# Kernel optimization log

Hardware: AMD Instinct MI355X
Metric: run time of the kernel (lower is better)

## Reference

```python
import jax, jax.numpy as jnp
import numpy as np

T, B, D, H = 256, 64, 1024, 1024  # seq_len, batch, input_dim, hidden_dim (= n_qubits)


def setup_inputs() -> dict:
    key = jax.random.key(0)
    ks = jax.random.split(key, 9)
    scale = 1.0 / np.sqrt(D + H)
    inp = {
        "inputs": jax.random.normal(ks[0], (T, B, D), dtype=jnp.float32),
        # nn.Linear weights (out=H wires, in=D+H) and biases, per gate
        "Wf": jax.random.normal(ks[1], (H, D + H), dtype=jnp.float32) * scale,
        "bf": jnp.zeros((H,), dtype=jnp.float32),
        "gbf": jnp.zeros((H,), dtype=jnp.float32),  # QLinearGate bias (init zeros)
        "Wi": jax.random.normal(ks[2], (H, D + H), dtype=jnp.float32) * scale,
        "bi": jnp.zeros((H,), dtype=jnp.float32),
        "gbi": jnp.zeros((H,), dtype=jnp.float32),
        "Wu": jax.random.normal(ks[3], (H, D + H), dtype=jnp.float32) * scale,
        "bu": jnp.zeros((H,), dtype=jnp.float32),
        "gbu": jnp.zeros((H,), dtype=jnp.float32),
        "Wo": jax.random.normal(ks[4], (H, D + H), dtype=jnp.float32) * scale,
        "bo": jnp.zeros((H,), dtype=jnp.float32),
        "gbo": jnp.zeros((H,), dtype=jnp.float32),
    }
    return inp


def reference(inputs, Wf, bf, gbf, Wi, bi, gbi, Wu, bu, gbu, Wo, bo, gbo):
    # QLinearGate: RY(theta)|0> -> <Z> = cos(theta); matmul with identity; add bias.
    def qgate(z, gb):
        return jnp.cos(z) + gb

    def step(carry, x):
        hx, cx = carry
        comb = jnp.concatenate([x, hx], axis=1)  # (B, D+H)
        f = jax.nn.sigmoid(qgate(comb @ Wf.T + bf, gbf))
        i = jax.nn.sigmoid(qgate(comb @ Wi.T + bi, gbi))
        g = jnp.tanh(qgate(comb @ Wu.T + bu, gbu))
        o = jax.nn.sigmoid(qgate(comb @ Wo.T + bo, gbo))
        cx = f * cx + i * g
        hx = o * jnp.tanh(cx)
        return (hx, cx), hx

    Bdim = inputs.shape[1]
    init = (jnp.zeros((Bdim, H), inputs.dtype), jnp.zeros((Bdim, H), inputs.dtype))
    (hx, cx), outputs = jax.lax.scan(step, init, inputs)
    return outputs, (hx, cx)
```

## Files before the change

kernel.cpp:

```cpp
#include <hip/hip_runtime.h>
#include <cmath>
#include <cstring>

constexpr int TT = 256;
constexpr int BB = 64;
constexpr int DD = 1024;
constexpr int HH = 1024;
constexpr int KK = DD + HH;
constexpr int NBLK = 256;
constexpr int NTHR = 512;
constexpr int CK = 64;
constexpr int NCHF = KK / CK;
constexpr int HPB = 4;

constexpr int WS_UINTS = TT * 8 * 16 + TT * 16;

__device__ __forceinline__ float sigm(float v) { return 1.0f / (1.0f + expf(-v)); }

__device__ __forceinline__ float qsum4(float x) {
  int v = __builtin_amdgcn_mov_dpp(__float_as_int(x), 0xB1, 0xF, 0xF, true);
  x += __int_as_float(v);
  v = __builtin_amdgcn_mov_dpp(__float_as_int(x), 0x4E, 0xF, 0xF, true);
  x += __int_as_float(v);
  return x;
}

__device__ __forceinline__ void gridbar(unsigned* ws, int t, int tid, int bid) {
  __syncthreads();
  if (tid == 0) {
    asm volatile("s_waitcnt vmcnt(0)" ::: "memory");
    unsigned* grp  = ws + (size_t)(t * 8 + (bid >> 5)) * 16;
    unsigned* done = ws + 32768 + (size_t)t * 16;
    unsigned old = __hip_atomic_fetch_add(grp, 1u, __ATOMIC_RELAXED, __HIP_MEMORY_SCOPE_AGENT);
    if (old == 31u)
      __hip_atomic_fetch_add(done, 1u, __ATOMIC_RELAXED, __HIP_MEMORY_SCOPE_AGENT);
    while (__hip_atomic_load(done, __ATOMIC_RELAXED, __HIP_MEMORY_SCOPE_AGENT) < 8u)
      __builtin_amdgcn_s_sleep(1);
    asm volatile("" ::: "memory");
  }
  __syncthreads();
}

__global__ void zero_ws(unsigned* p, int n) {
  int i = blockIdx.x * blockDim.x + threadIdx.x;
  if (i < n) p[i] = 0u;
}

__global__ __launch_bounds__(NTHR, 2)
void qlstm_fused3(const float* __restrict__ x,
                  const float* __restrict__ Wf, const float* __restrict__ bf, const float* __restrict__ gbf,
                  const float* __restrict__ Wi, const float* __restrict__ bi, const float* __restrict__ gbi,
                  const float* __restrict__ Wu, const float* __restrict__ bu, const float* __restrict__ gbu,
                  const float* __restrict__ Wo, const float* __restrict__ bo, const float* __restrict__ gbo,
                  float* __restrict__ out, unsigned* __restrict__ ws)
{
  __shared__ float lds[40960];
  float* const Wl   = lds;
  float* const cbA  = lds + 32768;
  float* const cbB  = lds + 36864;
  float* const zbuf = lds + 32768;

  const int tid  = threadIdx.x;
  const int lane = tid & 63;
  const int rg   = tid >> 6;
  const int cgp  = lane >> 4;
  const int kp   = lane & 15;
  const int srow = tid >> 3;
  const int sseg = tid & 7;
  const int bid  = blockIdx.x;
  const int h0   = bid * HPB;

  {
    const float* Wg[4] = {Wf, Wi, Wu, Wo};
    #pragma unroll
    for (int j = 0; j < 16; ++j) {
      const float4 w = *(const float4*)(Wg[j >> 2] + (size_t)(h0 + (j & 3)) * KK + tid * 4);
      *(float4*)&Wl[j * KK + tid * 4] = w;
    }
  }

  const int urow = tid >> 2;
  const int uhl  = tid & 3;
  const int hcell = h0 + uhl;
  float bfv = 0, gbfv = 0, biv = 0, gbiv = 0, buv = 0, gbuv = 0, bov = 0, gbov = 0;
  if (tid < 256) {
    bfv = bf[hcell]; gbfv = gbf[hcell];
    biv = bi[hcell]; gbiv = gbi[hcell];
    buv = bu[hcell]; gbuv = gbu[hcell];
    bov = bo[hcell]; gbov = gbo[hcell];
  }
  float cx = 0.0f, hxl = 0.0f;

  auto ld8 = [](const float* p) -> float2 {
    unsigned long long u = __hip_atomic_load((const unsigned long long*)(const void*)p,
                                             __ATOMIC_RELAXED, __HIP_MEMORY_SCOPE_AGENT);
    float2 r; __builtin_memcpy(&r, &u, 8); return r;
  };

  for (int t = 0; t < TT; ++t) {
    const int nch = (t == 0) ? (DD / CK) : NCHF;

    float acc[8][4];
    #pragma unroll
    for (int i = 0; i < 8; ++i)
      #pragma unroll
      for (int j = 0; j < 4; ++j) acc[i][j] = 0.0f;

    auto loadChunk = [&](int kc, float4& va, float4& vb) {
      const int k0 = kc * CK;
      if (k0 < DD) {
        const float* base = x + (size_t)t * BB * DD + (size_t)srow * DD + k0;
        va = *(const float4*)(base + sseg * 4);
        vb = *(const float4*)(base + 32 + sseg * 4);
      } else {
        const float* base = out + (size_t)(t - 1) * BB * HH + (size_t)srow * HH + (k0 - DD);
        const float2 a0 = ld8(base + sseg * 4);
        const float2 a1 = ld8(base + sseg * 4 + 2);
        const float2 b0 = ld8(base + 32 + sseg * 4);
        const float2 b1 = ld8(base + 32 + sseg * 4 + 2);
        va = {a0.x, a0.y, a1.x, a1.y};
        vb = {b0.x, b0.y, b1.x, b1.y};
      }
    };
    auto storeChunk = [&](float* cb, const float4 va, const float4 vb) {
      *(float4*)&cb[srow * CK + sseg * 4]      = va;
      *(float4*)&cb[srow * CK + 32 + sseg * 4] = vb;
    };

    float4 va, vb;
    loadChunk(0, va, vb);
    storeChunk(cbA, va, vb);
    loadChunk(1, va, vb);

    for (int kc = 0; kc < nch; ++kc) {
      float* const cbW = (kc & 1) ? cbA : cbB;
      float* const cbR = (kc & 1) ? cbB : cbA;
      if (kc + 1 < nch) storeChunk(cbW, va, vb);
      if (kc + 2 < nch) loadChunk(kc + 2, va, vb);

      const int cko = kc * CK;
      float4 cfr[8];
      #pragma unroll
      for (int i = 0; i < 8; ++i)
        cfr[i] = *(const float4*)&cbR[(rg * 8 + i) * CK + kp * 4];
      #pragma unroll
      for (int j = 0; j < 4; ++j) {
        const float4 w = *(const float4*)&Wl[(cgp * 4 + j) * KK + cko + kp * 4];
        #pragma unroll
        for (int i = 0; i < 8; ++i) {
          acc[i][j] = fmaf(cfr[i].x, w.x, acc[i][j]);
          acc[i][j] = fmaf(cfr[i].y, w.y, acc[i][j]);
          acc[i][j] = fmaf(cfr[i].z, w.z, acc[i][j]);
          acc[i][j] = fmaf(cfr[i].w, w.w, acc[i][j]);
        }
      }
    }

    #pragma unroll
    for (int i = 0; i < 8; ++i)
      #pragma unroll
      for (int j = 0; j < 4; ++j) acc[i][j] = qsum4(acc[i][j]);

    __syncthreads();
    if ((lane & 3) == 0) {
      const int kpg = (lane >> 2) & 3;
      #pragma unroll
      for (int i = 0; i < 8; ++i) {
        const float4 v = {acc[i][0], acc[i][1], acc[i][2], acc[i][3]};
        *(float4*)&zbuf[(size_t)((kpg * 64) + rg * 8 + i) * 16 + cgp * 4] = v;
      }
    }
    __syncthreads();

    if (tid < 256) {
      float zf = bfv, zi = biv, zu = buv, zo = bov;
      #pragma unroll
      for (int p = 0; p < 4; ++p) {
        const float* zr = &zbuf[(size_t)(p * 64 + urow) * 16];
        zf += zr[0 + uhl];
        zi += zr[4 + uhl];
        zu += zr[8 + uhl];
        zo += zr[12 + uhl];
      }
      const float fg = sigm(cosf(zf) + gbfv);
      const float ig = sigm(cosf(zi) + gbiv);
      const float gg = tanhf(cosf(zu) + gbuv);
      const float og = sigm(cosf(zo) + gbov);
      cx = fg * cx + ig * gg;
      const float hx = og * tanhf(cx);
      __hip_atomic_store(&out[(size_t)t * BB * HH + (size_t)urow * HH + hcell], hx,
                         __ATOMIC_RELAXED, __HIP_MEMORY_SCOPE_AGENT);
      hxl = hx;
    }

    gridbar(ws, t, tid, bid);
  }

  if (tid < 256) {
    float* hxout = out + (size_t)TT * BB * HH;
    float* cxout = hxout + (size_t)BB * HH;
    hxout[(size_t)urow * HH + hcell] = hxl;
    cxout[(size_t)urow * HH + hcell] = cx;
  }
}

extern "C" void kernel_launch(void* const* d_in, const int* in_sizes, int n_in,
                              void* d_out, int out_size, void* d_ws, size_t ws_size,
                              hipStream_t stream) {
  const float* x   = (const float*)d_in[0];
  const float* Wf  = (const float*)d_in[1];
  const float* bf_ = (const float*)d_in[2];
  const float* gbf = (const float*)d_in[3];
  const float* Wi  = (const float*)d_in[4];
  const float* bi_ = (const float*)d_in[5];
  const float* gbi = (const float*)d_in[6];
  const float* Wu  = (const float*)d_in[7];
  const float* bu_ = (const float*)d_in[8];
  const float* gbu = (const float*)d_in[9];
  const float* Wo  = (const float*)d_in[10];
  const float* bo_ = (const float*)d_in[11];
  const float* gbo = (const float*)d_in[12];
  float* out = (float*)d_out;
  unsigned* wsp = (unsigned*)d_ws;

  zero_ws<<<(WS_UINTS + 255) / 256, 256, 0, stream>>>(wsp, WS_UINTS);

  void* args[] = {&x, &Wf, &bf_, &gbf, &Wi, &bi_, &gbi, &Wu, &bu_, &gbu,
                  &Wo, &bo_, &gbo, &out, &wsp};
  hipLaunchCooperativeKernel((void*)qlstm_fused3, dim3(NBLK), dim3(NTHR),
                             args, 0, stream);
}
```

Measured before the change: 5.489 ms.

## Switch gate matmuls to split-bf16 MFMA with segmented input projection

Replaces the scalar FP32 FMA loop with bf16 MFMA 16x16x32 instructions. Weights and activations are split into hi and lo bf16 parts and combined with three MFMAs to keep accuracy close to FP32. Weights are stored swizzled in LDS. The input projection for 8 timesteps is computed ahead of the recurrent part and parked in workspace, so each barrier-separated step only does the hidden-state half of the K dimension. The cost is a larger LDS footprint (136 KB), which likely allows only one block per CU, plus extra workspace traffic and bf16-split rounding error.

```diff
diff --git a/kernel.cpp b/kernel.cpp
--- a/kernel.cpp
+++ b/kernel.cpp
@@ -6,23 +6,26 @@
 constexpr int BB = 64;
 constexpr int DD = 1024;
 constexpr int HH = 1024;
-constexpr int KK = DD + HH;
+constexpr int KK = 2048;
 constexpr int NBLK = 256;
 constexpr int NTHR = 512;
-constexpr int CK = 64;
-constexpr int NCHF = KK / CK;
+constexpr int SEG = 8;
+constexpr int NSEG = TT / SEG;
 constexpr int HPB = 4;
 
-constexpr int WS_UINTS = TT * 8 * 16 + TT * 16;
+constexpr int FLAG_UINTS = TT * 8 * 16 + TT * 16;
+
+typedef __attribute__((ext_vector_type(8))) short bf16x8;
+typedef __attribute__((ext_vector_type(4))) float f32x4;
 
 __device__ __forceinline__ float sigm(float v) { return 1.0f / (1.0f + expf(-v)); }
 
-__device__ __forceinline__ float qsum4(float x) {
-  int v = __builtin_amdgcn_mov_dpp(__float_as_int(x), 0xB1, 0xF, 0xF, true);
-  x += __int_as_float(v);
-  v = __builtin_amdgcn_mov_dpp(__float_as_int(x), 0x4E, 0xF, 0xF, true);
-  x += __int_as_float(v);
-  return x;
+__device__ __forceinline__ void split2(float c, short& hi, short& lo) {
+  unsigned u  = __float_as_uint(c);
+  unsigned uh = u & 0xFFFF0000u;
+  hi = (short)(uh >> 16);
+  float r = c - __uint_as_float(uh);
+  lo = (short)(__float_as_uint(r) >> 16);
 }
 
 __device__ __forceinline__ void gridbar(unsigned* ws, int t, int tid, int bid) {
@@ -47,35 +50,42 @@
 }
 
 __global__ __launch_bounds__(NTHR, 2)
-void qlstm_fused3(const float* __restrict__ x,
-                  const float* __restrict__ Wf, const float* __restrict__ bf, const float* __restrict__ gbf,
-                  const float* __restrict__ Wi, const float* __restrict__ bi, const float* __restrict__ gbi,
-                  const float* __restrict__ Wu, const float* __restrict__ bu, const float* __restrict__ gbu,
-                  const float* __restrict__ Wo, const float* __restrict__ bo, const float* __restrict__ gbo,
-                  float* __restrict__ out, unsigned* __restrict__ ws)
+void qlstm_mfma5(const float* __restrict__ x,
+                 const float* __restrict__ Wf, const float* __restrict__ bf, const float* __restrict__ gbf,
+                 const float* __restrict__ Wi, const float* __restrict__ bi, const float* __restrict__ gbi,
+                 const float* __restrict__ Wu, const float* __restrict__ bu, const float* __restrict__ gbu,
+                 const float* __restrict__ Wo, const float* __restrict__ bo, const float* __restrict__ gbo,
+                 float* __restrict__ out, unsigned* __restrict__ ws)
 {
-  __shared__ float lds[40960];
-  float* const Wl   = lds;
-  float* const cbA  = lds + 32768;
-  float* const cbB  = lds + 36864;
-  float* const zbuf = lds + 32768;
+  __shared__ __attribute__((aligned(16))) char smem[139264];
+  char*  const Whi  = smem;
+  char*  const Wlo  = smem + 65536;
+  float* const zbuf = (float*)(smem + 131072);
 
   const int tid  = threadIdx.x;
   const int lane = tid & 63;
-  const int rg   = tid >> 6;
-  const int cgp  = lane >> 4;
-  const int kp   = lane & 15;
-  const int srow = tid >> 3;
-  const int sseg = tid & 7;
+  const int wid  = tid >> 6;
+  const int m    = wid & 3;
+  const int p    = wid >> 2;
+  const int arow = lane & 15;
+  const int kseg = lane >> 4;
+  const int col  = lane & 15;
   const int bid  = blockIdx.x;
   const int h0   = bid * HPB;
 
+  float* const wsz = (float*)ws + FLAG_UINTS;
+
   {
     const float* Wg[4] = {Wf, Wi, Wu, Wo};
-    #pragma unroll
-    for (int j = 0; j < 16; ++j) {
-      const float4 w = *(const float4*)(Wg[j >> 2] + (size_t)(h0 + (j & 3)) * KK + tid * 4);
-      *(float4*)&Wl[j * KK + tid * 4] = w;
+    for (int u = tid; u < 4096; u += NTHR) {
+      const int c = u >> 8, s = u & 255;
+      const float* src = Wg[c >> 2] + (size_t)(h0 + (c & 3)) * KK + s * 8;
+      bf16x8 h8, l8;
+      #pragma unroll
+      for (int j = 0; j < 8; ++j) { short h, l; split2(src[j], h, l); h8[j] = h; l8[j] = l; }
+      const int addr = (c * 4096 + s * 16) ^ ((c & 7) << 4);
+      *(bf16x8*)(Whi + addr) = h8;
+      *(bf16x8*)(Wlo + addr) = l8;
     }
   }
 
@@ -91,109 +101,99 @@
   }
   float cx = 0.0f, hxl = 0.0f;
 
-  auto ld8 = [](const float* p) -> float2 {
-    unsigned long long u = __hip_atomic_load((const unsigned long long*)(const void*)p,
+  auto ld8 = [](const float* ptr) -> float2 {
+    unsigned long long u = __hip_atomic_load((const unsigned long long*)(const void*)ptr,
                                              __ATOMIC_RELAXED, __HIP_MEMORY_SCOPE_AGENT);
     float2 r; __builtin_memcpy(&r, &u, 8); return r;
   };
 
-  for (int t = 0; t < TT; ++t) {
-    const int nch = (t == 0) ? (DD / CK) : NCHF;
-
-    float acc[8][4];
+  auto kstep = [&](const float c[8], int kglob, f32x4& acc) {
+    bf16x8 ahi, alo;
     #pragma unroll
-    for (int i = 0; i < 8; ++i)
-      #pragma unroll
-      for (int j = 0; j < 4; ++j) acc[i][j] = 0.0f;
-
-    auto loadChunk = [&](int kc, float4& va, float4& vb) {
-      const int k0 = kc * CK;
-      if (k0 < DD) {
-        const float* base = x + (size_t)t * BB * DD + (size_t)srow * DD + k0;
-        va = *(const float4*)(base + sseg * 4);
-        vb = *(const float4*)(base + 32 + sseg * 4);
-      } else {
-        const float* base = out + (size_t)(t - 1) * BB * HH + (size_t)srow * HH + (k0 - DD);
-        const float2 a0 = ld8(base + sseg * 4);
-        const float2 a1 = ld8(base + sseg * 4 + 2);
-        const float2 b0 = ld8(base + 32 + sseg * 4);
-        const float2 b1 = ld8(base + 32 + sseg * 4 + 2);
-        va = {a0.x, a0.y, a1.x, a1.y};
-        vb = {b0.x, b0.y, b1.x, b1.y};
-      }
-    };
-    auto storeChunk = [&](float* cb, const float4 va, const float4 vb) {
-      *(float4*)&cb[srow * CK + sseg * 4]      = va;
-      *(float4*)&cb[srow * CK + 32 + sseg * 4] = vb;
-    };
-
-    float4 va, vb;
-    loadChunk(0, va, vb);
-    storeChunk(cbA, va, vb);
-    loadChunk(1, va, vb);
-
-    for (int kc = 0; kc < nch; ++kc) {
-      float* const cbW = (kc & 1) ? cbA : cbB;
-      float* const cbR = (kc & 1) ? cbB : cbA;
-      if (kc + 1 < nch) storeChunk(cbW, va, vb);
-      if (kc + 2 < nch) loadChunk(kc + 2, va, vb);
-
-      const int cko = kc * CK;
-      float4 cfr[8];
-      #pragma unroll
-      for (int i = 0; i < 8; ++i)
-        cfr[i] = *(const float4*)&cbR[(rg * 8 + i) * CK + kp * 4];
-      #pragma unroll
-      for (int j = 0; j < 4; ++j) {
-        const float4 w = *(const float4*)&Wl[(cgp * 4 + j) * KK + cko + kp * 4];
+    for (int j = 0; j < 8; ++j) { short h, l; split2(c[j], h, l); ahi[j] = h; alo[j] = l; }
+    const int ad = (col * 4096 + (kglob + kseg * 8) * 2) ^ ((col & 7) << 4);
+    const bf16x8 bhi = *(const bf16x8*)(Whi + ad);
+    const bf16x8 blo = *(const bf16x8*)(Wlo + ad);
+    acc = __builtin_amdgcn_mfma_f32_16x16x32_bf16(ahi, bhi, acc, 0, 0, 0);
+    acc = __builtin_amdgcn_mfma_f32_16x16x32_bf16(ahi, blo, acc, 0, 0, 0);
+    acc = __builtin_amdgcn_mfma_f32_16x16x32_bf16(alo, bhi, acc, 0, 0, 0);
+  };
+  auto writeC = [&](const f32x4 acc) {
+    *(f32x4*)&zbuf[((p * 4 + m) * 16 + col) * 16 + kseg * 4] = acc;
+  };
+
+  __syncthreads();
+
+  for (int seg = 0; seg < NSEG; ++seg) {
+    for (int s = 0; s < SEG; ++s) {
+      const int t = seg * SEG + s;
+      f32x4 acc = {0.f, 0.f, 0.f, 0.f};
+      const float* xrow = x + (size_t)t * BB * DD + (size_t)(m * 16 + arow) * DD;
+      #pragma unroll 4
+      for (int kb = 0; kb < 16; ++kb) {
+        const int k0 = (kb * 2 + p) * 32;
+        const float4 a0 = *(const float4*)(xrow + k0 + kseg * 8);
+        const float4 a1 = *(const float4*)(xrow + k0 + kseg * 8 + 4);
+        const float c[8] = {a0.x, a0.y, a0.z, a0.w, a1.x, a1.y, a1.z, a1.w};
+        kstep(c, k0, acc);
+      }
+      writeC(acc);
+      __syncthreads();
+      if (tid < 256) {
+        const int mr = urow >> 4, r = urow & 15;
+        float4 z4;
+        float* zz = (float*)&z4;
         #pragma unroll
-        for (int i = 0; i < 8; ++i) {
-          acc[i][j] = fmaf(cfr[i].x, w.x, acc[i][j]);
-          acc[i][j] = fmaf(cfr[i].y, w.y, acc[i][j]);
-          acc[i][j] = fmaf(cfr[i].z, w.z, acc[i][j]);
-          acc[i][j] = fmaf(cfr[i].w, w.w, acc[i][j]);
+        for (int g = 0; g < 4; ++g)
+          zz[g] = zbuf[((0 + mr) * 16 + g * 4 + uhl) * 16 + r]
+                + zbuf[((4 + mr) * 16 + g * 4 + uhl) * 16 + r];
+        *(float4*)&wsz[((size_t)(bid * SEG + s) * 256 + tid) * 4] = z4;
+      }
+      __syncthreads();
+    }
+
+    for (int s = 0; s < SEG; ++s) {
+      const int t = seg * SEG + s;
+      f32x4 acc = {0.f, 0.f, 0.f, 0.f};
+      if (t > 0) {
+        const float* hrow = out + (size_t)(t - 1) * BB * HH + (size_t)(m * 16 + arow) * HH;
+        #pragma unroll 4
+        for (int kb = 0; kb < 16; ++kb) {
+          const int k0 = (kb * 2 + p) * 32;
+          const float* bptr = hrow + k0 + kseg * 8;
+          const float2 q0 = ld8(bptr), q1 = ld8(bptr + 2), q2 = ld8(bptr + 4), q3 = ld8(bptr + 6);
+          const float c[8] = {q0.x, q0.y, q1.x, q1.y, q2.x, q2.y, q3.x, q3.y};
+          kstep(c, 1024 + k0, acc);
         }
       }
+      writeC(acc);
+      __syncthreads();
+
+      if (tid < 256) {
+        const float4 zx4 = *(const float4*)&wsz[((size_t)(bid * SEG + s) * 256 + tid) * 4];
+        const int mr = urow >> 4, r = urow & 15;
+        float zg[4];
+        #pragma unroll
+        for (int g = 0; g < 4; ++g)
+          zg[g] = zbuf[((0 + mr) * 16 + g * 4 + uhl) * 16 + r]
+                + zbuf[((4 + mr) * 16 + g * 4 + uhl) * 16 + r];
+        const float zf = bfv + zx4.x + zg[0];
+        const float zi = biv + zx4.y + zg[1];
+        const float zu = buv + zx4.z + zg[2];
+        const float zo = bov + zx4.w + zg[3];
+        const float fg = sigm(cosf(zf) + gbfv);
+        const float ig = sigm(cosf(zi) + gbiv);
+        const float gg = tanhf(cosf(zu) + gbuv);
+        const float og = sigm(cosf(zo) + gbov);
+        cx = fg * cx + ig * gg;
+        const float hx = og * tanhf(cx);
+        __hip_atomic_store(&out[(size_t)t * BB * HH + (size_t)urow * HH + hcell], hx,
+                           __ATOMIC_RELAXED, __HIP_MEMORY_SCOPE_AGENT);
+        hxl = hx;
+      }
+
+      gridbar(ws, t, tid, bid);
     }
-
-    #pragma unroll
-    for (int i = 0; i < 8; ++i)
-      #pragma unroll
-      for (int j = 0; j < 4; ++j) acc[i][j] = qsum4(acc[i][j]);
-
-    __syncthreads();
-    if ((lane & 3) == 0) {
-      const int kpg = (lane >> 2) & 3;
-      #pragma unroll
-      for (int i = 0; i < 8; ++i) {
-        const float4 v = {acc[i][0], acc[i][1], acc[i][2], acc[i][3]};
-        *(float4*)&zbuf[(size_t)((kpg * 64) + rg * 8 + i) * 16 + cgp * 4] = v;
-      }
-    }
-    __syncthreads();
-
-    if (tid < 256) {
-      float zf = bfv, zi = biv, zu = buv, zo = bov;
-      #pragma unroll
-      for (int p = 0; p < 4; ++p) {
-        const float* zr = &zbuf[(size_t)(p * 64 + urow) * 16];
-        zf += zr[0 + uhl];
-        zi += zr[4 + uhl];
-        zu += zr[8 + uhl];
-        zo += zr[12 + uhl];
-      }
-      const float fg = sigm(cosf(zf) + gbfv);
-      const float ig = sigm(cosf(zi) + gbiv);
-      const float gg = tanhf(cosf(zu) + gbuv);
-      const float og = sigm(cosf(zo) + gbov);
-      cx = fg * cx + ig * gg;
-      const float hx = og * tanhf(cx);
-      __hip_atomic_store(&out[(size_t)t * BB * HH + (size_t)urow * HH + hcell], hx,
-                         __ATOMIC_RELAXED, __HIP_MEMORY_SCOPE_AGENT);
-      hxl = hx;
-    }
-
-    gridbar(ws, t, tid, bid);
   }
 
   if (tid < 256) {
@@ -223,10 +223,10 @@
   float* out = (float*)d_out;
   unsigned* wsp = (unsigned*)d_ws;
 
-  zero_ws<<<(WS_UINTS + 255) / 256, 256, 0, stream>>>(wsp, WS_UINTS);
+  zero_ws<<<(FLAG_UINTS + 255) / 256, 256, 0, stream>>>(wsp, FLAG_UINTS);
 
   void* args[] = {&x, &Wf, &bf_, &gbf, &Wi, &bi_, &gbi, &Wu, &bu_, &gbu,
                   &Wo, &bo_, &gbo, &out, &wsp};
-  hipLaunchCooperativeKernel((void*)qlstm_fused3, dim3(NBLK), dim3(NTHR),
+  hipLaunchCooperativeKernel((void*)qlstm_mfma5, dim3(NBLK), dim3(NTHR),
                              args, 0, stream);
 }
```

Result: slower. 6.662 ms (+21.4%).
